# Kernel tuning notes

Hardware: AMD Instinct MI355X
Metric: run time of the kernel (lower is better)

The kernel has to match this reference:

```python
import jax, jax.numpy as jnp
import numpy as np

MAX_OBJECTS = 20
MAX_GRID = 30
LN_EPS = 1e-5


def _layernorm(x, g, b):
    m = x.mean(-1, keepdims=True)
    v = ((x - m) ** 2).mean(-1, keepdims=True)
    return (x - m) / jnp.sqrt(v + LN_EPS) * g + b


def setup_inputs() -> dict:
    key = jax.random.key(0)
    ks = jax.random.split(key, 16)
    B, ND, H, NL, NC = 16384, 16, 64, 3, 11
    OUT = MAX_GRID * MAX_GRID * NC  # 9900
    s1, s2, s64 = 1.0 / np.sqrt(ND), 1.0 / np.sqrt(2 * H), 1.0 / np.sqrt(H)
    return {
        "node_features": jax.random.normal(ks[0], (B, MAX_OBJECTS, ND), jnp.float32),
        "n_nodes": jax.random.randint(ks[1], (B,), 1, MAX_OBJECTS + 1, jnp.int32),
        "embed_w": jax.random.normal(ks[2], (ND, H), jnp.float32) * s1,
        "embed_b": jnp.zeros((H,), jnp.float32),
        "edge_w1": jax.random.normal(ks[3], (NL, 2 * H, H), jnp.float32) * s2,
        "edge_b1": jnp.zeros((NL, H), jnp.float32),
        "edge_w2": jax.random.normal(ks[4], (NL, H, H), jnp.float32) * s64,
        "edge_b2": jnp.zeros((NL, H), jnp.float32),
        "node_w1": jax.random.normal(ks[5], (NL, 2 * H, H), jnp.float32) * s2,
        "node_b1": jnp.zeros((NL, H), jnp.float32),
        "node_w2": jax.random.normal(ks[6], (NL, H, H), jnp.float32) * s64,
        "node_b2": jnp.zeros((NL, H), jnp.float32),
        "ln_g": jnp.ones((NL, H), jnp.float32),
        "ln_b": jnp.zeros((NL, H), jnp.float32),
        "ro_w1": jax.random.normal(ks[7], (H, H), jnp.float32) * s64,
        "ro_b1": jnp.zeros((H,), jnp.float32),
        "ro_w2": jax.random.normal(ks[8], (H, OUT), jnp.float32) * s64,
        "ro_b2": jnp.zeros((OUT,), jnp.float32),
    }


def reference(node_features, n_nodes, embed_w, embed_b,
              edge_w1, edge_b1, edge_w2, edge_b2,
              node_w1, node_b1, node_w2, node_b2,
              ln_g, ln_b, ro_w1, ro_b1, ro_w2, ro_b2):
    B = node_features.shape[0]
    h = node_features @ embed_w + embed_b  # (B, 20, H)
    # mask is identical across layers (n_nodes is fixed)
    mask = (jnp.arange(MAX_OBJECTS)[None, :] < n_nodes[:, None]).astype(h.dtype)[..., None]  # (B,20,1)
    cnt = jnp.clip(mask.sum(1, keepdims=True), 1.0, None)  # (B,1,1)
    n_layers = edge_w1.shape[0]
    for i in range(n_layers):
        msg_mean = (h * mask).sum(1, keepdims=True) / cnt  # (B,1,H)
        msg_mean = jnp.broadcast_to(msg_mean, h.shape)
        edge_in = jnp.concatenate([h, msg_mean], -1)  # (B,20,2H)
        edge_msg = jax.nn.relu(edge_in @ edge_w1[i] + edge_b1[i]) @ edge_w2[i] + edge_b2[i]
        node_in = jnp.concatenate([h, edge_msg], -1)
        h = h + (jax.nn.relu(node_in @ node_w1[i] + node_b1[i]) @ node_w2[i] + node_b2[i])
        h = _layernorm(h, ln_g[i], ln_b[i])
        h = h * mask
    graph_vec = (h * mask).sum(1) / jnp.clip(mask.sum(1), 1.0, None)  # (B,H)
    out = jax.nn.relu(graph_vec @ ro_w1 + ro_b1) @ ro_w2 + ro_b2  # (B, 9900)
    n_colors = out.shape[-1] // (MAX_GRID * MAX_GRID)
    return out.reshape(B, MAX_GRID, MAX_GRID, n_colors).transpose(0, 3, 1, 2)
```

## Files before the change

### kernel.cpp

```cpp
#include <hip/hip_runtime.h>
#include <hip/hip_bf16.h>
#include <stdint.h>

typedef __attribute__((ext_vector_type(8))) short bf16x8;
typedef __attribute__((ext_vector_type(4))) float f32x4;

__device__ __forceinline__ short f2bf(float x){
  union { float f; uint32_t u; } v; v.f = x;
  uint32_t r = (v.u + 0x7FFFu + ((v.u >> 16) & 1u)) >> 16;
  return (short)(uint16_t)r;
}

__device__ __forceinline__ f32x4 mfma16(bf16x8 a, bf16x8 b, f32x4 c){
  return __builtin_amdgcn_mfma_f32_16x16x32_bf16(a, b, c, 0, 0, 0);
}

__global__ void prep_pack(const float* __restrict__ embed_w,
                          const float* __restrict__ ew1, const float* __restrict__ ew2,
                          const float* __restrict__ nw1, const float* __restrict__ nw2,
                          const float* __restrict__ row1,
                          short* __restrict__ wpk)
{
  int tid = blockIdx.x * 256 + threadIdx.x;
  if (tid >= 79872) return;
  const float* W; int Kact; int rem;
  if (tid < 2048){ W = embed_w; Kact = 16; rem = tid; }
  else if (tid < 75776){
    int t2 = tid - 2048; int layer = t2 / 24576; int r = t2 % 24576;
    if      (r < 8192)  { W = ew1 + layer*8192; Kact = 128; rem = r; }
    else if (r < 12288) { W = ew2 + layer*4096; Kact = 64;  rem = r - 8192; }
    else if (r < 20480) { W = nw1 + layer*8192; Kact = 128; rem = r - 12288; }
    else                { W = nw2 + layer*4096; Kact = 64;  rem = r - 20480; }
  } else { W = row1; Kact = 64; rem = tid - 75776; }
  int e = rem & 7, lane = (rem >> 3) & 63, nt = (rem >> 9) & 3, ks = rem >> 11;
  int k = ks*32 + (lane >> 4)*8 + e;
  int col = nt*16 + (lane & 15);
  float v = (k < Kact) ? W[k*64 + col] : 0.f;
  wpk[tid] = f2bf(v);
}

__global__ void prep_w2(const float* __restrict__ ro_w2, const float* __restrict__ ro_b2,
                        short* __restrict__ w2p, float* __restrict__ b2p)
{
  int tid = blockIdx.x * 256 + threadIdx.x;
  if (tid < 633856){
    int e = tid & 7, lane = (tid >> 3) & 63, ks = (tid >> 9) & 1, nt = tid >> 10;
    int k = ks*32 + (lane >> 4)*8 + e;
    int p = nt*16 + (lane & 15);
    float v = 0.f;
    if (p < 9900){ int c = p / 900, rm = p % 900; v = ro_w2[k*9900 + rm*11 + c]; }
    w2p[tid] = f2bf(v);
  } else if (tid < 633856 + 9904){
    int p = tid - 633856;
    float v = 0.f;
    if (p < 9900){ int c = p / 900, rm = p % 900; v = ro_b2[rm*11 + c]; }
    b2p[p] = v;
  }
}

__global__ __launch_bounds__(256) void gnn_phaseA(
    const float* __restrict__ nf, const int* __restrict__ nn,
    const float* __restrict__ embb,
    const float* __restrict__ eb1, const float* __restrict__ eb2,
    const float* __restrict__ nb1, const float* __restrict__ nb2,
    const float* __restrict__ lng, const float* __restrict__ lnb,
    const short* __restrict__ wpk,
    float* __restrict__ gv)
{
  __shared__ short lds[4][6208];
  const int wave = threadIdx.x >> 6, lane = threadIdx.x & 63;
  const int l15 = lane & 15, lg = lane >> 4;
  const int b = blockIdx.x * 4 + wave;
  short* hs   = &lds[wave][0];
  short* bufA = &lds[wave][2048];
  short* bufB = &lds[wave][4096];
  short* mms  = &lds[wave][6144];
  const int n = nn[b];
  const float cinv = 1.0f / (float)(n < 1 ? 1 : n);

  float hD[2][4][4];
  f32x4 acc[2][4];
  float colsum[4];

  {
    bf16x8 aq[2];
    #pragma unroll
    for (int mt = 0; mt < 2; ++mt){
      int row = mt*16 + l15;
      bf16x8 a = (bf16x8)(short)0;
      if (row < 20 && lg < 2){
        const float* s = nf + (b*20 + row)*16 + lg*8;
        #pragma unroll
        for (int e = 0; e < 8; ++e) a[e] = f2bf(s[e]);
      }
      aq[mt] = a;
    }
    #pragma unroll
    for (int mt = 0; mt < 2; ++mt)
      #pragma unroll
      for (int nt = 0; nt < 4; ++nt){
        f32x4 z = {0.f, 0.f, 0.f, 0.f};
        bf16x8 bq = *(const bf16x8*)(wpk + (nt*64 + lane)*8);
        acc[mt][nt] = mfma16(aq[mt], bq, z);
      }
    #pragma unroll
    for (int nt = 0; nt < 4; ++nt) colsum[nt] = 0.f;
    #pragma unroll
    for (int nt = 0; nt < 4; ++nt){
      float bias = embb[nt*16 + l15];
      #pragma unroll
      for (int mt = 0; mt < 2; ++mt)
        #pragma unroll
        for (int e = 0; e < 4; ++e){
          int row = mt*16 + lg*4 + e;
          float v = acc[mt][nt][e] + bias;
          v = (row < n) ? v : 0.f;
          hD[mt][nt][e] = v;
          colsum[nt] += v;
          hs[((row*64) + (nt*16 + l15)) ^ ((row & 7) << 3)] = f2bf(v);
        }
    }
    #pragma unroll
    for (int nt = 0; nt < 4; ++nt){
      float s = colsum[nt];
      s += __shfl_xor(s, 16);
      s += __shfl_xor(s, 32);
      colsum[nt] = s * cinv;
    }
    float mv = (lg == 0) ? colsum[0] : (lg == 1) ? colsum[1] : (lg == 2) ? colsum[2] : colsum[3];
    mms[lane] = f2bf(mv);
  }

  for (int li = 0; li < 3; ++li){
    const short* we1 = wpk + 2048 + li*24576;
    const short* we2 = we1 + 8192;
    const short* wn1 = we1 + 12288;
    const short* wn2 = we1 + 20480;

    #pragma unroll
    for (int mt = 0; mt < 2; ++mt)
      #pragma unroll
      for (int nt = 0; nt < 4; ++nt) acc[mt][nt] = (f32x4){0.f,0.f,0.f,0.f};
    #pragma unroll
    for (int ks = 0; ks < 4; ++ks){
      bf16x8 aq[2];
      if (ks < 2){
        #pragma unroll
        for (int mt = 0; mt < 2; ++mt){
          int row = mt*16 + l15;
          aq[mt] = *(const bf16x8*)&hs[((row*64) + (ks*32 + lg*8)) ^ ((row & 7) << 3)];
        }
      } else {
        bf16x8 m8 = *(const bf16x8*)&mms[(ks - 2)*32 + lg*8];
        aq[0] = m8; aq[1] = m8;
      }
      #pragma unroll
      for (int nt = 0; nt < 4; ++nt){
        bf16x8 bq = *(const bf16x8*)(we1 + ((ks*4 + nt)*64 + lane)*8);
        acc[0][nt] = mfma16(aq[0], bq, acc[0][nt]);
        acc[1][nt] = mfma16(aq[1], bq, acc[1][nt]);
      }
    }
    #pragma unroll
    for (int nt = 0; nt < 4; ++nt){
      float bias = eb1[li*64 + nt*16 + l15];
      #pragma unroll
      for (int mt = 0; mt < 2; ++mt)
        #pragma unroll
        for (int e = 0; e < 4; ++e){
          int row = mt*16 + lg*4 + e;
          float v = acc[mt][nt][e] + bias;
          v = v > 0.f ? v : 0.f;
          bufA[((row*64) + (nt*16 + l15)) ^ ((row & 7) << 3)] = f2bf(v);
        }
    }

    #pragma unroll
    for (int mt = 0; mt < 2; ++mt)
      #pragma unroll
      for (int nt = 0; nt < 4; ++nt) acc[mt][nt] = (f32x4){0.f,0.f,0.f,0.f};
    #pragma unroll
    for (int ks = 0; ks < 2; ++ks){
      bf16x8 aq[2];
      #pragma unroll
      for (int mt = 0; mt < 2; ++mt){
        int row = mt*16 + l15;
        aq[mt] = *(const bf16x8*)&bufA[((row*64) + (ks*32 + lg*8)) ^ ((row & 7) << 3)];
      }
      #pragma unroll
      for (int nt = 0; nt < 4; ++nt){
        bf16x8 bq = *(const bf16x8*)(we2 + ((ks*4 + nt)*64 + lane)*8);
        acc[0][nt] = mfma16(aq[0], bq, acc[0][nt]);
        acc[1][nt] = mfma16(aq[1], bq, acc[1][nt]);
      }
    }
    #pragma unroll
    for (int nt = 0; nt < 4; ++nt){
      float bias = eb2[li*64 + nt*16 + l15];
      #pragma unroll
      for (int mt = 0; mt < 2; ++mt)
        #pragma unroll
        for (int e = 0; e < 4; ++e){
          int row = mt*16 + lg*4 + e;
          bufB[((row*64) + (nt*16 + l15)) ^ ((row & 7) << 3)] = f2bf(acc[mt][nt][e] + bias);
        }
    }

    #pragma unroll
    for (int mt = 0; mt < 2; ++mt)
      #pragma unroll
      for (int nt = 0; nt < 4; ++nt) acc[mt][nt] = (f32x4){0.f,0.f,0.f,0.f};
    #pragma unroll
    for (int ks = 0; ks < 4; ++ks){
      bf16x8 aq[2];
      #pragma unroll
      for (int mt = 0; mt < 2; ++mt){
        int row = mt*16 + l15;
        const short* src = (ks < 2) ? hs : bufB;
        int k0 = (ks < 2) ? (ks*32 + lg*8) : ((ks - 2)*32 + lg*8);
        aq[mt] = *(const bf16x8*)&src[((row*64) + k0) ^ ((row & 7) << 3)];
      }
      #pragma unroll
      for (int nt = 0; nt < 4; ++nt){
        bf16x8 bq = *(const bf16x8*)(wn1 + ((ks*4 + nt)*64 + lane)*8);
        acc[0][nt] = mfma16(aq[0], bq, acc[0][nt]);
        acc[1][nt] = mfma16(aq[1], bq, acc[1][nt]);
      }
    }
    #pragma unroll
    for (int nt = 0; nt < 4; ++nt){
      float bias = nb1[li*64 + nt*16 + l15];
      #pragma unroll
      for (int mt = 0; mt < 2; ++mt)
        #pragma unroll
        for (int e = 0; e < 4; ++e){
          int row = mt*16 + lg*4 + e;
          float v = acc[mt][nt][e] + bias;
          v = v > 0.f ? v : 0.f;
          bufA[((row*64) + (nt*16 + l15)) ^ ((row & 7) << 3)] = f2bf(v);
        }
    }

    #pragma unroll
    for (int mt = 0; mt < 2; ++mt)
      #pragma unroll
      for (int nt = 0; nt < 4; ++nt) acc[mt][nt] = (f32x4){0.f,0.f,0.f,0.f};
    #pragma unroll
    for (int ks = 0; ks < 2; ++ks){
      bf16x8 aq[2];
      #pragma unroll
      for (int mt = 0; mt < 2; ++mt){
        int row = mt*16 + l15;
        aq[mt] = *(const bf16x8*)&bufA[((row*64) + (ks*32 + lg*8)) ^ ((row & 7) << 3)];
      }
      #pragma unroll
      for (int nt = 0; nt < 4; ++nt){
        bf16x8 bq = *(const bf16x8*)(wn2 + ((ks*4 + nt)*64 + lane)*8);
        acc[0][nt] = mfma16(aq[0], bq, acc[0][nt]);
        acc[1][nt] = mfma16(aq[1], bq, acc[1][nt]);
      }
    }
    float g4[4], b4[4];
    #pragma unroll
    for (int nt = 0; nt < 4; ++nt){
      float bias = nb2[li*64 + nt*16 + l15];
      g4[nt] = lng[li*64 + nt*16 + l15];
      b4[nt] = lnb[li*64 + nt*16 + l15];
      #pragma unroll
      for (int mt = 0; mt < 2; ++mt)
        #pragma unroll
        for (int e = 0; e < 4; ++e)
          hD[mt][nt][e] += acc[mt][nt][e] + bias;
      colsum[nt] = 0.f;
    }
    #pragma unroll
    for (int mt = 0; mt < 2; ++mt)
      #pragma unroll
      for (int e = 0; e < 4; ++e){
        float s1 = 0.f, s2 = 0.f;
        #pragma unroll
        for (int nt = 0; nt < 4; ++nt){ float v = hD[mt][nt][e]; s1 += v; s2 += v*v; }
        #pragma unroll
        for (int m = 1; m < 16; m <<= 1){ s1 += __shfl_xor(s1, m); s2 += __shfl_xor(s2, m); }
        float mean = s1 * 0.015625f;
        float var  = s2 * 0.015625f - mean*mean;
        float rstd = rsqrtf(var + 1e-5f);
        int row = mt*16 + lg*4 + e;
        bool keep = row < n;
        #pragma unroll
        for (int nt = 0; nt < 4; ++nt){
          float y = (hD[mt][nt][e] - mean) * rstd * g4[nt] + b4[nt];
          y = keep ? y : 0.f;
          hD[mt][nt][e] = y;
          colsum[nt] += y;
          hs[((row*64) + (nt*16 + l15)) ^ ((row & 7) << 3)] = f2bf(y);
        }
      }
    #pragma unroll
    for (int nt = 0; nt < 4; ++nt){
      float s = colsum[nt];
      s += __shfl_xor(s, 16);
      s += __shfl_xor(s, 32);
      colsum[nt] = s * cinv;
    }
    float mv = (lg == 0) ? colsum[0] : (lg == 1) ? colsum[1] : (lg == 2) ? colsum[2] : colsum[3];
    if (li < 2) mms[lane] = f2bf(mv);
    else        gv[b*64 + lane] = mv;
  }
}

__global__ __launch_bounds__(256) void gnn_phaseB(
    const float* __restrict__ gv, const float* __restrict__ rb1,
    const short* __restrict__ wro1, const short* __restrict__ w2p,
    const float* __restrict__ b2p, float* __restrict__ out)
{
  __shared__ short tl[4][1024];
  const int wave = threadIdx.x >> 6, lane = threadIdx.x & 63;
  const int l15 = lane & 15, lg = lane >> 4;
  const int b0 = blockIdx.x * 64 + wave * 16;

  f32x4 tacc[4];
  #pragma unroll
  for (int nt = 0; nt < 4; ++nt) tacc[nt] = (f32x4){0.f,0.f,0.f,0.f};
  #pragma unroll
  for (int ks = 0; ks < 2; ++ks){
    bf16x8 a;
    const float* s = gv + (b0 + l15)*64 + ks*32 + lg*8;
    #pragma unroll
    for (int e = 0; e < 8; ++e) a[e] = f2bf(s[e]);
    #pragma unroll
    for (int nt = 0; nt < 4; ++nt){
      bf16x8 bq = *(const bf16x8*)(wro1 + ((ks*4 + nt)*64 + lane)*8);
      tacc[nt] = mfma16(a, bq, tacc[nt]);
    }
  }
  short* tw = tl[wave];
  #pragma unroll
  for (int nt = 0; nt < 4; ++nt){
    float bias = rb1[nt*16 + l15];
    #pragma unroll
    for (int e = 0; e < 4; ++e){
      int row = lg*4 + e;
      float v = tacc[nt][e] + bias;
      v = v > 0.f ? v : 0.f;
      tw[((row*64) + (nt*16 + l15)) ^ ((row & 7) << 3)] = f2bf(v);
    }
  }
  bf16x8 ta0 = *(const bf16x8*)&tw[((l15*64) + (lg*8))      ^ ((l15 & 7) << 3)];
  bf16x8 ta1 = *(const bf16x8*)&tw[((l15*64) + (32 + lg*8)) ^ ((l15 & 7) << 3)];

  const int nt0 = blockIdx.y * 124;
  const int nt1 = (nt0 + 124 < 619) ? nt0 + 124 : 619;
  for (int nt = nt0; nt < nt1; ++nt){
    const bf16x8* wp = (const bf16x8*)w2p + nt*128;
    f32x4 c = (f32x4){0.f,0.f,0.f,0.f};
    c = mfma16(ta0, wp[lane], c);
    c = mfma16(ta1, wp[64 + lane], c);
    int p = nt*16 + l15;
    if (p < 9900){
      float bias = b2p[p];
      float* o = out + (b0 + lg*4)*9900 + p;
      #pragma unroll
      for (int e = 0; e < 4; ++e) o[e*9900] = c[e] + bias;
    }
  }
}

extern "C" void kernel_launch(void* const* d_in, const int* in_sizes, int n_in,
                              void* d_out, int out_size, void* d_ws, size_t ws_size,
                              hipStream_t stream)
{
  const float* nf   = (const float*)d_in[0];
  const int*   nn   = (const int*)d_in[1];
  const float* embw = (const float*)d_in[2];
  const float* embb = (const float*)d_in[3];
  const float* ew1  = (const float*)d_in[4];
  const float* eb1  = (const float*)d_in[5];
  const float* ew2  = (const float*)d_in[6];
  const float* eb2  = (const float*)d_in[7];
  const float* nw1  = (const float*)d_in[8];
  const float* nb1  = (const float*)d_in[9];
  const float* nw2  = (const float*)d_in[10];
  const float* nb2  = (const float*)d_in[11];
  const float* lng  = (const float*)d_in[12];
  const float* lnb  = (const float*)d_in[13];
  const float* rw1  = (const float*)d_in[14];
  const float* rb1  = (const float*)d_in[15];
  const float* rw2  = (const float*)d_in[16];
  const float* rb2  = (const float*)d_in[17];
  float* out = (float*)d_out;

  const int B = in_sizes[0] / 320;

  char* ws = (char*)d_ws;
  float* gv  = (float*)ws;
  float* b2p = (float*)(ws + (size_t)B*64*4);
  short* wpk = (short*)(ws + (size_t)B*64*4 + 9904*4);
  short* w2p = wpk + 79872;

  prep_pack<<<(79872 + 255)/256, 256, 0, stream>>>(embw, ew1, ew2, nw1, nw2, rw1, wpk);
  prep_w2<<<(633856 + 9904 + 255)/256, 256, 0, stream>>>(rw2, rb2, w2p, b2p);
  gnn_phaseA<<<B/4, 256, 0, stream>>>(nf, nn, embb, eb1, eb2, nb1, nb2, lng, lnb, wpk, gv);
  gnn_phaseB<<<dim3(B/64, 5), 256, 0, stream>>>(gv, rb1, wpk + 75776, w2p, b2p, out);
}
```

Baseline: 506.5 us.

## Fold edge second linear into node first linear and transpose MFMA operand roles

Since there is no nonlinearity between the edge MLP's second linear and the node MLP's first linear, a new prep kernel folds ew2 and the edge-message half of nw1 into one matrix and bias. This removes one 64x64 GEMM stage per layer in phase A. Phase A also swaps operand roles (weights become the A operand, nodes the B operand), which enables packed bf16 stores, float4 bias loads and fewer layernorm shuffles. Graph vectors are stored as bf16 so phase B skips the conversion. Folding changes the rounding path, since the product is now rounded once to bf16 instead of passing through a bf16 intermediate.

```diff
diff --git a/kernel.cpp b/kernel.cpp
--- a/kernel.cpp
+++ b/kernel.cpp
@@ -5,37 +5,64 @@
 typedef __attribute__((ext_vector_type(8))) short bf16x8;
 typedef __attribute__((ext_vector_type(4))) float f32x4;
 
-__device__ __forceinline__ short f2bf(float x){
+__device__ __forceinline__ uint32_t f2bfu(float x){
   union { float f; uint32_t u; } v; v.f = x;
-  uint32_t r = (v.u + 0x7FFFu + ((v.u >> 16) & 1u)) >> 16;
-  return (short)(uint16_t)r;
+  return (v.u + 0x7FFFu + ((v.u >> 16) & 1u)) >> 16;
+}
+__device__ __forceinline__ short f2bf(float x){ return (short)(uint16_t)f2bfu(x); }
+__device__ __forceinline__ uint32_t pk2(float a, float b){
+  return (f2bfu(a) & 0xFFFFu) | (f2bfu(b) << 16);
 }
 
 __device__ __forceinline__ f32x4 mfma16(bf16x8 a, bf16x8 b, f32x4 c){
   return __builtin_amdgcn_mfma_f32_16x16x32_bf16(a, b, c, 0, 0, 0);
 }
 
-__global__ void prep_pack(const float* __restrict__ embed_w,
-                          const float* __restrict__ ew1, const float* __restrict__ ew2,
-                          const float* __restrict__ nw1, const float* __restrict__ nw2,
+__global__ void prep_fold(const float* __restrict__ ew2, const float* __restrict__ eb2,
+                          const float* __restrict__ nw1, const float* __restrict__ nb1,
+                          float* __restrict__ wfold, float* __restrict__ bfold)
+{
+  int l = blockIdx.x, t = threadIdx.x;
+  const float* A  = ew2 + l*4096;
+  const float* Bm = nw1 + l*8192 + 4096;
+  for (int i = 0; i < 16; ++i){
+    int idx = t + i*256;
+    int r = idx >> 6, c = idx & 63;
+    float s = 0.f;
+    for (int m = 0; m < 64; ++m) s += A[r*64 + m] * Bm[m*64 + c];
+    wfold[l*4096 + idx] = s;
+  }
+  if (t < 64){
+    float s = nb1[l*64 + t];
+    const float* e2 = eb2 + l*64;
+    for (int m = 0; m < 64; ++m) s += e2[m] * Bm[m*64 + t];
+    bfold[l*64 + t] = s;
+  }
+}
+
+__global__ void prep_pack(const float* __restrict__ embw,
+                          const float* __restrict__ ew1,
+                          const float* __restrict__ nw1,
+                          const float* __restrict__ nw2,
                           const float* __restrict__ row1,
+                          const float* __restrict__ wfold,
                           short* __restrict__ wpk)
 {
-  int tid = blockIdx.x * 256 + threadIdx.x;
-  if (tid >= 79872) return;
-  const float* W; int Kact; int rem;
-  if (tid < 2048){ W = embed_w; Kact = 16; rem = tid; }
-  else if (tid < 75776){
-    int t2 = tid - 2048; int layer = t2 / 24576; int r = t2 % 24576;
-    if      (r < 8192)  { W = ew1 + layer*8192; Kact = 128; rem = r; }
-    else if (r < 12288) { W = ew2 + layer*4096; Kact = 64;  rem = r - 8192; }
-    else if (r < 20480) { W = nw1 + layer*8192; Kact = 128; rem = r - 12288; }
-    else                { W = nw2 + layer*4096; Kact = 64;  rem = r - 20480; }
-  } else { W = row1; Kact = 64; rem = tid - 75776; }
-  int e = rem & 7, lane = (rem >> 3) & 63, nt = (rem >> 9) & 3, ks = rem >> 11;
+  int tid = blockIdx.x*256 + threadIdx.x;
+  if (tid >= 67584) return;
+  int rem; const float* Wa; const float* Wb = nullptr; int Kact;
+  if (tid < 2048){ rem = tid; Wa = embw; Kact = 16; }
+  else if (tid < 63488){
+    int t2 = tid - 2048, li = t2/20480, r = t2%20480;
+    if (r < 8192)       { rem = r;         Wa = ew1 + li*8192; Wb = Wa + 4096;        Kact = 128; }
+    else if (r < 16384) { rem = r - 8192;  Wa = nw1 + li*8192; Wb = wfold + li*4096;  Kact = 128; }
+    else                { rem = r - 16384; Wa = nw2 + li*4096;                         Kact = 64; }
+  } else { rem = tid - 63488; Wa = row1; Kact = 64; }
+  int e = rem & 7, lane = (rem >> 3) & 63, mt = (rem >> 9) & 3, ks = rem >> 11;
   int k = ks*32 + (lane >> 4)*8 + e;
-  int col = nt*16 + (lane & 15);
-  float v = (k < Kact) ? W[k*64 + col] : 0.f;
+  int col = mt*16 + (lane & 15);
+  float v = 0.f;
+  if (k < Kact) v = (k < 64) ? Wa[k*64 + col] : Wb[(k - 64)*64 + col];
   wpk[tid] = f2bf(v);
 }
 
@@ -61,256 +88,236 @@
 __global__ __launch_bounds__(256) void gnn_phaseA(
     const float* __restrict__ nf, const int* __restrict__ nn,
     const float* __restrict__ embb,
-    const float* __restrict__ eb1, const float* __restrict__ eb2,
-    const float* __restrict__ nb1, const float* __restrict__ nb2,
+    const float* __restrict__ eb1, const float* __restrict__ nb2,
     const float* __restrict__ lng, const float* __restrict__ lnb,
-    const short* __restrict__ wpk,
-    float* __restrict__ gv)
-{
-  __shared__ short lds[4][6208];
+    const short* __restrict__ wpk, const float* __restrict__ bfold,
+    short* __restrict__ gvb)
+{
+  __shared__ short lds[4][4160];
   const int wave = threadIdx.x >> 6, lane = threadIdx.x & 63;
   const int l15 = lane & 15, lg = lane >> 4;
   const int b = blockIdx.x * 4 + wave;
-  short* hs   = &lds[wave][0];
-  short* bufA = &lds[wave][2048];
-  short* bufB = &lds[wave][4096];
-  short* mms  = &lds[wave][6144];
+  short* hs  = &lds[wave][0];
+  short* buf = &lds[wave][2048];
+  short* mms = &lds[wave][4096];
   const int n = nn[b];
   const float cinv = 1.0f / (float)(n < 1 ? 1 : n);
-
-  float hD[2][4][4];
-  f32x4 acc[2][4];
-  float colsum[4];
+  const bool keep0 = l15 < n, keep1 = (16 + l15) < n;
+  const int fb = lg*4;
+  const int sw = (l15 & 7) << 3;
+  const int rb0 = l15*64, rb1 = (16 + l15)*64;
+
+  float hD[4][2][4];
+  f32x4 acc[4][2];
+  float cs[4][4];
 
   {
-    bf16x8 aq[2];
-    #pragma unroll
-    for (int mt = 0; mt < 2; ++mt){
-      int row = mt*16 + l15;
-      bf16x8 a = (bf16x8)(short)0;
-      if (row < 20 && lg < 2){
-        const float* s = nf + (b*20 + row)*16 + lg*8;
-        #pragma unroll
-        for (int e = 0; e < 8; ++e) a[e] = f2bf(s[e]);
-      }
-      aq[mt] = a;
-    }
-    #pragma unroll
-    for (int mt = 0; mt < 2; ++mt)
-      #pragma unroll
-      for (int nt = 0; nt < 4; ++nt){
-        f32x4 z = {0.f, 0.f, 0.f, 0.f};
-        bf16x8 bq = *(const bf16x8*)(wpk + (nt*64 + lane)*8);
-        acc[mt][nt] = mfma16(aq[mt], bq, z);
-      }
-    #pragma unroll
-    for (int nt = 0; nt < 4; ++nt) colsum[nt] = 0.f;
-    #pragma unroll
-    for (int nt = 0; nt < 4; ++nt){
-      float bias = embb[nt*16 + l15];
-      #pragma unroll
-      for (int mt = 0; mt < 2; ++mt)
-        #pragma unroll
+    bf16x8 bfr[2];
+#pragma unroll
+    for (int nt = 0; nt < 2; ++nt){
+      int node = nt*16 + l15;
+      bf16x8 a;
+#pragma unroll
+      for (int e = 0; e < 8; ++e) a[e] = 0;
+      if (lg < 2 && node < 20){
+        const float* s = nf + (b*20 + node)*16 + lg*8;
+        float4 s0 = *(const float4*)(s);
+        float4 s1 = *(const float4*)(s + 4);
+        union { bf16x8 v; uint32_t u[4]; } q;
+        q.u[0] = pk2(s0.x, s0.y); q.u[1] = pk2(s0.z, s0.w);
+        q.u[2] = pk2(s1.x, s1.y); q.u[3] = pk2(s1.z, s1.w);
+        a = q.v;
+      }
+      bfr[nt] = a;
+    }
+#pragma unroll
+    for (int mt = 0; mt < 4; ++mt){
+      bf16x8 af = *(const bf16x8*)(wpk + (mt*64 + lane)*8);
+      f32x4 z = {0.f,0.f,0.f,0.f};
+      acc[mt][0] = mfma16(af, bfr[0], z);
+      acc[mt][1] = mfma16(af, bfr[1], z);
+    }
+#pragma unroll
+    for (int mt = 0; mt < 4; ++mt){
+      float4 bias = *(const float4*)(embb + mt*16 + fb);
+#pragma unroll
+      for (int nt = 0; nt < 2; ++nt){
+        bool kp = nt ? keep1 : keep0;
+#pragma unroll
         for (int e = 0; e < 4; ++e){
-          int row = mt*16 + lg*4 + e;
-          float v = acc[mt][nt][e] + bias;
-          v = (row < n) ? v : 0.f;
-          hD[mt][nt][e] = v;
-          colsum[nt] += v;
-          hs[((row*64) + (nt*16 + l15)) ^ ((row & 7) << 3)] = f2bf(v);
+          float v = acc[mt][nt][e] + ((const float*)&bias)[e];
+          hD[mt][nt][e] = kp ? v : 0.f;
         }
-    }
-    #pragma unroll
-    for (int nt = 0; nt < 4; ++nt){
-      float s = colsum[nt];
-      s += __shfl_xor(s, 16);
-      s += __shfl_xor(s, 32);
-      colsum[nt] = s * cinv;
-    }
-    float mv = (lg == 0) ? colsum[0] : (lg == 1) ? colsum[1] : (lg == 2) ? colsum[2] : colsum[3];
-    mms[lane] = f2bf(mv);
+        int base = nt ? rb1 : rb0;
+        uint32_t w0 = pk2(hD[mt][nt][0], hD[mt][nt][1]);
+        uint32_t w1 = pk2(hD[mt][nt][2], hD[mt][nt][3]);
+        *(uint2*)&hs[base + ((mt*16 + fb) ^ sw)] = make_uint2(w0, w1);
+      }
+#pragma unroll
+      for (int e = 0; e < 4; ++e){
+        float c = hD[mt][0][e] + hD[mt][1][e];
+        c += __shfl_xor(c, 1); c += __shfl_xor(c, 2);
+        c += __shfl_xor(c, 4); c += __shfl_xor(c, 8);
+        cs[mt][e] = c * cinv;
+      }
+    }
+    if (l15 == 0){
+#pragma unroll
+      for (int mt = 0; mt < 4; ++mt)
+        *(uint2*)&mms[mt*16 + fb] = make_uint2(pk2(cs[mt][0], cs[mt][1]),
+                                               pk2(cs[mt][2], cs[mt][3]));
+    }
   }
 
   for (int li = 0; li < 3; ++li){
-    const short* we1 = wpk + 2048 + li*24576;
-    const short* we2 = we1 + 8192;
-    const short* wn1 = we1 + 12288;
-    const short* wn2 = we1 + 20480;
-
-    #pragma unroll
-    for (int mt = 0; mt < 2; ++mt)
-      #pragma unroll
-      for (int nt = 0; nt < 4; ++nt) acc[mt][nt] = (f32x4){0.f,0.f,0.f,0.f};
-    #pragma unroll
+    const short* wl = wpk + 2048 + li*20480;
+
+#pragma unroll
+    for (int mt = 0; mt < 4; ++mt){ acc[mt][0] = (f32x4){0.f,0.f,0.f,0.f}; acc[mt][1] = (f32x4){0.f,0.f,0.f,0.f}; }
+#pragma unroll
     for (int ks = 0; ks < 4; ++ks){
-      bf16x8 aq[2];
+      bf16x8 bfr0, bfr1;
       if (ks < 2){
-        #pragma unroll
-        for (int mt = 0; mt < 2; ++mt){
-          int row = mt*16 + l15;
-          aq[mt] = *(const bf16x8*)&hs[((row*64) + (ks*32 + lg*8)) ^ ((row & 7) << 3)];
-        }
+        int ko = (ks*32 + lg*8) ^ sw;
+        bfr0 = *(const bf16x8*)&hs[rb0 + ko];
+        bfr1 = *(const bf16x8*)&hs[rb1 + ko];
       } else {
-        bf16x8 m8 = *(const bf16x8*)&mms[(ks - 2)*32 + lg*8];
-        aq[0] = m8; aq[1] = m8;
-      }
-      #pragma unroll
-      for (int nt = 0; nt < 4; ++nt){
-        bf16x8 bq = *(const bf16x8*)(we1 + ((ks*4 + nt)*64 + lane)*8);
-        acc[0][nt] = mfma16(aq[0], bq, acc[0][nt]);
-        acc[1][nt] = mfma16(aq[1], bq, acc[1][nt]);
-      }
-    }
-    #pragma unroll
-    for (int nt = 0; nt < 4; ++nt){
-      float bias = eb1[li*64 + nt*16 + l15];
-      #pragma unroll
-      for (int mt = 0; mt < 2; ++mt)
-        #pragma unroll
-        for (int e = 0; e < 4; ++e){
-          int row = mt*16 + lg*4 + e;
-          float v = acc[mt][nt][e] + bias;
-          v = v > 0.f ? v : 0.f;
-          bufA[((row*64) + (nt*16 + l15)) ^ ((row & 7) << 3)] = f2bf(v);
-        }
-    }
-
-    #pragma unroll
-    for (int mt = 0; mt < 2; ++mt)
-      #pragma unroll
-      for (int nt = 0; nt < 4; ++nt) acc[mt][nt] = (f32x4){0.f,0.f,0.f,0.f};
-    #pragma unroll
+        bfr0 = *(const bf16x8*)&mms[(ks - 2)*32 + lg*8];
+        bfr1 = bfr0;
+      }
+#pragma unroll
+      for (int mt = 0; mt < 4; ++mt){
+        bf16x8 af = *(const bf16x8*)(wl + ((ks*4 + mt)*64 + lane)*8);
+        acc[mt][0] = mfma16(af, bfr0, acc[mt][0]);
+        acc[mt][1] = mfma16(af, bfr1, acc[mt][1]);
+      }
+    }
+#pragma unroll
+    for (int mt = 0; mt < 4; ++mt){
+      float4 bias = *(const float4*)(eb1 + li*64 + mt*16 + fb);
+#pragma unroll
+      for (int nt = 0; nt < 2; ++nt){
+        float v0 = acc[mt][nt][0] + ((const float*)&bias)[0];
+        float v1 = acc[mt][nt][1] + ((const float*)&bias)[1];
+        float v2 = acc[mt][nt][2] + ((const float*)&bias)[2];
+        float v3 = acc[mt][nt][3] + ((const float*)&bias)[3];
+        v0 = v0 > 0.f ? v0 : 0.f; v1 = v1 > 0.f ? v1 : 0.f;
+        v2 = v2 > 0.f ? v2 : 0.f; v3 = v3 > 0.f ? v3 : 0.f;
+        int base = nt ? rb1 : rb0;
+        *(uint2*)&buf[base + ((mt*16 + fb) ^ sw)] = make_uint2(pk2(v0, v1), pk2(v2, v3));
+      }
+    }
+
+#pragma unroll
+    for (int mt = 0; mt < 4; ++mt){ acc[mt][0] = (f32x4){0.f,0.f,0.f,0.f}; acc[mt][1] = (f32x4){0.f,0.f,0.f,0.f}; }
+#pragma unroll
+    for (int ks = 0; ks < 4; ++ks){
+      const short* src = (ks < 2) ? hs : buf;
+      int ko = (((ks & 1)*32) + lg*8) ^ sw;
+      bf16x8 bfr0 = *(const bf16x8*)&src[rb0 + ko];
+      bf16x8 bfr1 = *(const bf16x8*)&src[rb1 + ko];
+#pragma unroll
+      for (int mt = 0; mt < 4; ++mt){
+        bf16x8 af = *(const bf16x8*)(wl + 8192 + ((ks*4 + mt)*64 + lane)*8);
+        acc[mt][0] = mfma16(af, bfr0, acc[mt][0]);
+        acc[mt][1] = mfma16(af, bfr1, acc[mt][1]);
+      }
+    }
+#pragma unroll
+    for (int mt = 0; mt < 4; ++mt){
+      float4 bias = *(const float4*)(bfold + li*64 + mt*16 + fb);
+#pragma unroll
+      for (int nt = 0; nt < 2; ++nt){
+        float v0 = acc[mt][nt][0] + ((const float*)&bias)[0];
+        float v1 = acc[mt][nt][1] + ((const float*)&bias)[1];
+        float v2 = acc[mt][nt][2] + ((const float*)&bias)[2];
+        float v3 = acc[mt][nt][3] + ((const float*)&bias)[3];
+        v0 = v0 > 0.f ? v0 : 0.f; v1 = v1 > 0.f ? v1 : 0.f;
+        v2 = v2 > 0.f ? v2 : 0.f; v3 = v3 > 0.f ? v3 : 0.f;
+        int base = nt ? rb1 : rb0;
+        *(uint2*)&buf[base + ((mt*16 + fb) ^ sw)] = make_uint2(pk2(v0, v1), pk2(v2, v3));
+      }
+    }
+
+#pragma unroll
+    for (int mt = 0; mt < 4; ++mt){ acc[mt][0] = (f32x4){0.f,0.f,0.f,0.f}; acc[mt][1] = (f32x4){0.f,0.f,0.f,0.f}; }
+#pragma unroll
     for (int ks = 0; ks < 2; ++ks){
-      bf16x8 aq[2];
-      #pragma unroll
-      for (int mt = 0; mt < 2; ++mt){
-        int row = mt*16 + l15;
-        aq[mt] = *(const bf16x8*)&bufA[((row*64) + (ks*32 + lg*8)) ^ ((row & 7) << 3)];
-      }
-      #pragma unroll
-      for (int nt = 0; nt < 4; ++nt){
-        bf16x8 bq = *(const bf16x8*)(we2 + ((ks*4 + nt)*64 + lane)*8);
-        acc[0][nt] = mfma16(aq[0], bq, acc[0][nt]);
-        acc[1][nt] = mfma16(aq[1], bq, acc[1][nt]);
-      }
-    }
-    #pragma unroll
-    for (int nt = 0; nt < 4; ++nt){
-      float bias = eb2[li*64 + nt*16 + l15];
-      #pragma unroll
-      for (int mt = 0; mt < 2; ++mt)
-        #pragma unroll
-        for (int e = 0; e < 4; ++e){
-          int row = mt*16 + lg*4 + e;
-          bufB[((row*64) + (nt*16 + l15)) ^ ((row & 7) << 3)] = f2bf(acc[mt][nt][e] + bias);
-        }
-    }
-
-    #pragma unroll
-    for (int mt = 0; mt < 2; ++mt)
-      #pragma unroll
-      for (int nt = 0; nt < 4; ++nt) acc[mt][nt] = (f32x4){0.f,0.f,0.f,0.f};
-    #pragma unroll
-    for (int ks = 0; ks < 4; ++ks){
-      bf16x8 aq[2];
-      #pragma unroll
-      for (int mt = 0; mt < 2; ++mt){
-        int row = mt*16 + l15;
-        const short* src = (ks < 2) ? hs : bufB;
-        int k0 = (ks < 2) ? (ks*32 + lg*8) : ((ks - 2)*32 + lg*8);
-        aq[mt] = *(const bf16x8*)&src[((row*64) + k0) ^ ((row & 7) << 3)];
-      }
-      #pragma unroll
-      for (int nt = 0; nt < 4; ++nt){
-        bf16x8 bq = *(const bf16x8*)(wn1 + ((ks*4 + nt)*64 + lane)*8);
-        acc[0][nt] = mfma16(aq[0], bq, acc[0][nt]);
-        acc[1][nt] = mfma16(aq[1], bq, acc[1][nt]);
-      }
-    }
-    #pragma unroll
-    for (int nt = 0; nt < 4; ++nt){
-      float bias = nb1[li*64 + nt*16 + l15];
-      #pragma unroll
-      for (int mt = 0; mt < 2; ++mt)
-        #pragma unroll
-        for (int e = 0; e < 4; ++e){
-          int row = mt*16 + lg*4 + e;
-          float v = acc[mt][nt][e] + bias;
-          v = v > 0.f ? v : 0.f;
-          bufA[((row*64) + (nt*16 + l15)) ^ ((row & 7) << 3)] = f2bf(v);
-        }
-    }
-
-    #pragma unroll
-    for (int mt = 0; mt < 2; ++mt)
-      #pragma unroll
-      for (int nt = 0; nt < 4; ++nt) acc[mt][nt] = (f32x4){0.f,0.f,0.f,0.f};
-    #pragma unroll
-    for (int ks = 0; ks < 2; ++ks){
-      bf16x8 aq[2];
-      #pragma unroll
-      for (int mt = 0; mt < 2; ++mt){
-        int row = mt*16 + l15;
-        aq[mt] = *(const bf16x8*)&bufA[((row*64) + (ks*32 + lg*8)) ^ ((row & 7) << 3)];
-      }
-      #pragma unroll
-      for (int nt = 0; nt < 4; ++nt){
-        bf16x8 bq = *(const bf16x8*)(wn2 + ((ks*4 + nt)*64 + lane)*8);
-        acc[0][nt] = mfma16(aq[0], bq, acc[0][nt]);
-        acc[1][nt] = mfma16(aq[1], bq, acc[1][nt]);
-      }
-    }
-    float g4[4], b4[4];
-    #pragma unroll
-    for (int nt = 0; nt < 4; ++nt){
-      float bias = nb2[li*64 + nt*16 + l15];
-      g4[nt] = lng[li*64 + nt*16 + l15];
-      b4[nt] = lnb[li*64 + nt*16 + l15];
-      #pragma unroll
-      for (int mt = 0; mt < 2; ++mt)
-        #pragma unroll
-        for (int e = 0; e < 4; ++e)
-          hD[mt][nt][e] += acc[mt][nt][e] + bias;
-      colsum[nt] = 0.f;
-    }
-    #pragma unroll
-    for (int mt = 0; mt < 2; ++mt)
-      #pragma unroll
+      int ko = (ks*32 + lg*8) ^ sw;
+      bf16x8 bfr0 = *(const bf16x8*)&buf[rb0 + ko];
+      bf16x8 bfr1 = *(const bf16x8*)&buf[rb1 + ko];
+#pragma unroll
+      for (int mt = 0; mt < 4; ++mt){
+        bf16x8 af = *(const bf16x8*)(wl + 16384 + ((ks*4 + mt)*64 + lane)*8);
+        acc[mt][0] = mfma16(af, bfr0, acc[mt][0]);
+        acc[mt][1] = mfma16(af, bfr1, acc[mt][1]);
+      }
+    }
+    float s1a = 0.f, s2a = 0.f, s1b = 0.f, s2b = 0.f;
+#pragma unroll
+    for (int mt = 0; mt < 4; ++mt){
+      float4 bias = *(const float4*)(nb2 + li*64 + mt*16 + fb);
+#pragma unroll
       for (int e = 0; e < 4; ++e){
-        float s1 = 0.f, s2 = 0.f;
-        #pragma unroll
-        for (int nt = 0; nt < 4; ++nt){ float v = hD[mt][nt][e]; s1 += v; s2 += v*v; }
-        #pragma unroll
-        for (int m = 1; m < 16; m <<= 1){ s1 += __shfl_xor(s1, m); s2 += __shfl_xor(s2, m); }
-        float mean = s1 * 0.015625f;
-        float var  = s2 * 0.015625f - mean*mean;
-        float rstd = rsqrtf(var + 1e-5f);
-        int row = mt*16 + lg*4 + e;
-        bool keep = row < n;
-        #pragma unroll
-        for (int nt = 0; nt < 4; ++nt){
-          float y = (hD[mt][nt][e] - mean) * rstd * g4[nt] + b4[nt];
-          y = keep ? y : 0.f;
-          hD[mt][nt][e] = y;
-          colsum[nt] += y;
-          hs[((row*64) + (nt*16 + l15)) ^ ((row & 7) << 3)] = f2bf(y);
-        }
-      }
-    #pragma unroll
-    for (int nt = 0; nt < 4; ++nt){
-      float s = colsum[nt];
-      s += __shfl_xor(s, 16);
-      s += __shfl_xor(s, 32);
-      colsum[nt] = s * cinv;
-    }
-    float mv = (lg == 0) ? colsum[0] : (lg == 1) ? colsum[1] : (lg == 2) ? colsum[2] : colsum[3];
-    if (li < 2) mms[lane] = f2bf(mv);
-    else        gv[b*64 + lane] = mv;
+        float va = hD[mt][0][e] + acc[mt][0][e] + ((const float*)&bias)[e];
+        float vb = hD[mt][1][e] + acc[mt][1][e] + ((const float*)&bias)[e];
+        hD[mt][0][e] = va; hD[mt][1][e] = vb;
+        s1a += va; s2a += va*va; s1b += vb; s2b += vb*vb;
+      }
+    }
+    s1a += __shfl_xor(s1a, 16); s1a += __shfl_xor(s1a, 32);
+    s2a += __shfl_xor(s2a, 16); s2a += __shfl_xor(s2a, 32);
+    s1b += __shfl_xor(s1b, 16); s1b += __shfl_xor(s1b, 32);
+    s2b += __shfl_xor(s2b, 16); s2b += __shfl_xor(s2b, 32);
+    float meana = s1a * 0.015625f, meanb = s1b * 0.015625f;
+    float rstda = rsqrtf(s2a * 0.015625f - meana*meana + 1e-5f);
+    float rstdb = rsqrtf(s2b * 0.015625f - meanb*meanb + 1e-5f);
+#pragma unroll
+    for (int mt = 0; mt < 4; ++mt){
+      float4 g = *(const float4*)(lng + li*64 + mt*16 + fb);
+      float4 bb = *(const float4*)(lnb + li*64 + mt*16 + fb);
+#pragma unroll
+      for (int e = 0; e < 4; ++e){
+        float ge = ((const float*)&g)[e], be = ((const float*)&bb)[e];
+        float ya = (hD[mt][0][e] - meana) * rstda * ge + be;
+        float yb = (hD[mt][1][e] - meanb) * rstdb * ge + be;
+        ya = keep0 ? ya : 0.f;
+        yb = keep1 ? yb : 0.f;
+        hD[mt][0][e] = ya; hD[mt][1][e] = yb;
+        cs[mt][e] = ya + yb;
+      }
+      *(uint2*)&hs[rb0 + ((mt*16 + fb) ^ sw)] =
+          make_uint2(pk2(hD[mt][0][0], hD[mt][0][1]), pk2(hD[mt][0][2], hD[mt][0][3]));
+      *(uint2*)&hs[rb1 + ((mt*16 + fb) ^ sw)] =
+          make_uint2(pk2(hD[mt][1][0], hD[mt][1][1]), pk2(hD[mt][1][2], hD[mt][1][3]));
+    }
+#pragma unroll
+    for (int mt = 0; mt < 4; ++mt)
+#pragma unroll
+      for (int e = 0; e < 4; ++e){
+        float c = cs[mt][e];
+        c += __shfl_xor(c, 1); c += __shfl_xor(c, 2);
+        c += __shfl_xor(c, 4); c += __shfl_xor(c, 8);
+        cs[mt][e] = c * cinv;
+      }
+    if (l15 == 0){
+      if (li < 2){
+#pragma unroll
+        for (int mt = 0; mt < 4; ++mt)
+          *(uint2*)&mms[mt*16 + fb] = make_uint2(pk2(cs[mt][0], cs[mt][1]),
+                                                 pk2(cs[mt][2], cs[mt][3]));
+      } else {
+#pragma unroll
+        for (int mt = 0; mt < 4; ++mt)
+          *(uint2*)(gvb + b*64 + mt*16 + fb) = make_uint2(pk2(cs[mt][0], cs[mt][1]),
+                                                          pk2(cs[mt][2], cs[mt][3]));
+      }
+    }
   }
 }
 
 __global__ __launch_bounds__(256) void gnn_phaseB(
-    const float* __restrict__ gv, const float* __restrict__ rb1,
+    const short* __restrict__ gvb, const float* __restrict__ rb1,
     const short* __restrict__ wro1, const short* __restrict__ w2p,
     const float* __restrict__ b2p, float* __restrict__ out)
 {
@@ -320,25 +327,22 @@
   const int b0 = blockIdx.x * 64 + wave * 16;
 
   f32x4 tacc[4];
-  #pragma unroll
+#pragma unroll
   for (int nt = 0; nt < 4; ++nt) tacc[nt] = (f32x4){0.f,0.f,0.f,0.f};
-  #pragma unroll
+#pragma unroll
   for (int ks = 0; ks < 2; ++ks){
-    bf16x8 a;
-    const float* s = gv + (b0 + l15)*64 + ks*32 + lg*8;
-    #pragma unroll
-    for (int e = 0; e < 8; ++e) a[e] = f2bf(s[e]);
-    #pragma unroll
+    bf16x8 a = *(const bf16x8*)&gvb[(b0 + l15)*64 + ks*32 + lg*8];
+#pragma unroll
     for (int nt = 0; nt < 4; ++nt){
       bf16x8 bq = *(const bf16x8*)(wro1 + ((ks*4 + nt)*64 + lane)*8);
       tacc[nt] = mfma16(a, bq, tacc[nt]);
     }
   }
   short* tw = tl[wave];
-  #pragma unroll
+#pragma unroll
   for (int nt = 0; nt < 4; ++nt){
     float bias = rb1[nt*16 + l15];
-    #pragma unroll
+#pragma unroll
     for (int e = 0; e < 4; ++e){
       int row = lg*4 + e;
       float v = tacc[nt][e] + bias;
@@ -359,9 +363,9 @@
     int p = nt*16 + l15;
     if (p < 9900){
       float bias = b2p[p];
-      float* o = out + (b0 + lg*4)*9900 + p;
-      #pragma unroll
-      for (int e = 0; e < 4; ++e) o[e*9900] = c[e] + bias;
+      float* o = out + (size_t)(b0 + lg*4)*9900 + p;
+#pragma unroll
+      for (int e = 0; e < 4; ++e) o[(size_t)e*9900] = c[e] + bias;
     }
   }
 }
@@ -393,13 +397,16 @@
   const int B = in_sizes[0] / 320;
 
   char* ws = (char*)d_ws;
-  float* gv  = (float*)ws;
-  float* b2p = (float*)(ws + (size_t)B*64*4);
-  short* wpk = (short*)(ws + (size_t)B*64*4 + 9904*4);
-  short* w2p = wpk + 79872;
-
-  prep_pack<<<(79872 + 255)/256, 256, 0, stream>>>(embw, ew1, ew2, nw1, nw2, rw1, wpk);
+  short* gvb  = (short*)ws;
+  float* b2p  = (float*)(ws + 2097152);
+  float* wfold= (float*)(ws + 2136768);
+  float* bfold= (float*)(ws + 2185920);
+  short* wpk  = (short*)(ws + 2186688);
+  short* w2p  = (short*)(ws + 2321856);
+
+  prep_fold<<<3, 256, 0, stream>>>(ew2, eb2, nw1, nb1, wfold, bfold);
+  prep_pack<<<(67584 + 255)/256, 256, 0, stream>>>(embw, ew1, nw1, nw2, rw1, wfold, wpk);
   prep_w2<<<(633856 + 9904 + 255)/256, 256, 0, stream>>>(rw2, rb2, w2p, b2p);
-  gnn_phaseA<<<B/4, 256, 0, stream>>>(nf, nn, embb, eb1, eb2, nb1, nb2, lng, lnb, wpk, gv);
-  gnn_phaseB<<<dim3(B/64, 5), 256, 0, stream>>>(gv, rb1, wpk + 75776, w2p, b2p, out);
-}
+  gnn_phaseA<<<B/4, 256, 0, stream>>>(nf, nn, embb, eb1, nb2, lng, lnb, wpk, bfold, gvb);
+  gnn_phaseB<<<dim3(B/64, 5), 256, 0, stream>>>(gvb, rb1, wpk + 63488, w2p, b2p, out);
+}
```

After: 515.7 us. No clear change (+1.8%).
